# Kernel tuning notes

Hardware: AMD Instinct MI355X
Metric: run time of the kernel (lower is better)

Reference implementation:

```python
import jax, jax.numpy as jnp
import numpy as np

B, N, D, H = 256, 32768, 1024, 16
DH = D // H

def setup_inputs() -> dict:
    key = jax.random.key(0)
    ks = jax.random.split(key, 6)
    scale = 1.0 / np.sqrt(D)  # xavier-ish scale for weights
    return {
        "q": jax.random.normal(ks[0], (B, D), jnp.float32),
        "k": jax.random.normal(ks[1], (N, D), jnp.float32),
        "v": jax.random.normal(ks[2], (N, D), jnp.float32),
        "W_q": jax.random.normal(ks[3], (D, D), jnp.float32) * scale,
        "W_k": jax.random.normal(ks[4], (D, D), jnp.float32) * scale,
        "W_v": jax.random.normal(ks[5], (D, D), jnp.float32) * scale,
    }

def reference(q, k, v, W_q, W_k, W_v):
    # nn.Linear(x) = x @ W.T (no bias)
    qh = (q @ W_q.T).reshape(B, H, DH)   # [B,H,dh]
    kh = (k @ W_k.T).reshape(N, H, DH)   # [N,H,dh]
    vh = (v @ W_v.T).reshape(N, H, DH)   # [N,H,dh]
    inv_sqrt_dh = 1.0 / np.sqrt(DH).astype(np.float32)
    # decode-style cross attention: single query per (head, batch) over N keys
    score = jnp.einsum('bhd,nhd->hbn', qh, kh) * inv_sqrt_dh  # [H,B,N]
    weights = jax.nn.softmax(score, axis=-1)                   # [H,B,N]
    # dropout is identity in eval mode
    context = jnp.einsum('hbn,nhd->bhd', weights, vh)          # [B,H,dh]
    return context.reshape(B, D)
```

## Files before the change

### kernel.cpp

```cpp
#include <hip/hip_runtime.h>
#include <hip/hip_bf16.h>

#define B_  256
#define N_  32768
#define D_  1024
#define H_  16
#define DH_ 64
#define KSPLIT 16
#define STRIPE (N_ / KSPLIT)

typedef __attribute__((ext_vector_type(8))) short bf16x8;
typedef __attribute__((ext_vector_type(4))) float f32x4;

static __device__ __forceinline__ short f2bf(float f) {
    union { __hip_bfloat16 h; short s; } u;
    u.h = __float2bfloat16(f);
    return u.s;
}

__global__ __launch_bounds__(256)
void f2b_kernel(const float* __restrict__ in, short* __restrict__ out, int n4)
{
    int i = blockIdx.x * 256 + threadIdx.x;
    if (i < n4) {
        float4 v = ((const float4*)in)[i];
        ((short4*)out)[i] = make_short4(f2bf(v.x), f2bf(v.y), f2bf(v.z), f2bf(v.w));
    }
}

template<bool SWAP>
__global__ __launch_bounds__(256, 2)
void gemm_hybrid(const float* __restrict__ P, const short* __restrict__ Qb,
                 short* __restrict__ C, int MP, int MQ, int K, int ldc, float alpha)
{
    __shared__ __align__(16) short Pf[128 * 32];
    __shared__ __align__(16) short Qs[128 * 32];

    const int tid  = threadIdx.x;
    const int wave = tid >> 6;
    const int lane = tid & 63;
    const int quad = lane >> 4;
    const int l16  = lane & 15;

    const int gp = MP >> 7, gq = MQ >> 7;
    const int bid = blockIdx.x;
    int bp, bq;
    if (gp >= 8) {
        int xcd = bid & 7, w = bid >> 3, sp = gp >> 3;
        bp = xcd * sp + w / gq;
        bq = w % gq;
    } else { bp = bid / gq; bq = bid % gq; }

    const int wm = (wave & 1) * 64;
    const int wn = (wave >> 1) * 64;

    f32x4 acc[4][4];
#pragma unroll
    for (int i = 0; i < 4; ++i)
#pragma unroll
        for (int j = 0; j < 4; ++j) acc[i][j] = (f32x4){0.f, 0.f, 0.f, 0.f};

    for (int kt = 0; kt < K; kt += 32) {
        __syncthreads();
#pragma unroll
        for (int it = 0; it < 4; ++it) {
            int s = it * 256 + tid, r = s >> 3, c4 = s & 7;
            float4 v = *(const float4*)(P + (size_t)(bp * 128 + r) * K + kt + c4 * 4);
            *(short4*)&Pf[r * 32 + c4 * 4] =
                make_short4(f2bf(v.x), f2bf(v.y), f2bf(v.z), f2bf(v.w));
        }
#pragma unroll
        for (int it = 0; it < 2; ++it) {
            int s = it * 256 + tid, r = s >> 2, c8 = s & 3;
            *(bf16x8*)&Qs[r * 32 + c8 * 8] =
                *(const bf16x8*)(Qb + (size_t)(bq * 128 + r) * K + kt + c8 * 8);
        }
        __syncthreads();

        const short* LA = SWAP ? Qs : Pf;
        const short* LB = SWAP ? Pf : Qs;
        bf16x8 af[4], bf[4];
#pragma unroll
        for (int mi = 0; mi < 4; ++mi)
            af[mi] = *(const bf16x8*)&LA[(wm + mi * 16 + l16) * 32 + quad * 8];
#pragma unroll
        for (int ni = 0; ni < 4; ++ni)
            bf[ni] = *(const bf16x8*)&LB[(wn + ni * 16 + l16) * 32 + quad * 8];
#pragma unroll
        for (int mi = 0; mi < 4; ++mi)
#pragma unroll
            for (int ni = 0; ni < 4; ++ni)
                acc[mi][ni] = __builtin_amdgcn_mfma_f32_16x16x32_bf16(
                    af[mi], bf[ni], acc[mi][ni], 0, 0, 0);
    }

    const int rb = (SWAP ? bq : bp) * 128;
    const int cb = (SWAP ? bp : bq) * 128;
#pragma unroll
    for (int mi = 0; mi < 4; ++mi)
#pragma unroll
        for (int ni = 0; ni < 4; ++ni)
#pragma unroll
            for (int reg = 0; reg < 4; ++reg) {
                int r = rb + wm + mi * 16 + quad * 4 + reg;
                int c = cb + wn + ni * 16 + l16;
                C[(size_t)r * ldc + c] = f2bf(acc[mi][ni][reg] * alpha);
            }
}

__global__ __launch_bounds__(256, 2)
void attn_kernel(const short* __restrict__ qh, const short* __restrict__ kh,
                 const short* __restrict__ vhT, float* __restrict__ partO,
                 float* __restrict__ partM, float* __restrict__ partL)
{
    const int st = blockIdx.x, qb2 = blockIdx.y, h = blockIdx.z;
    const int tid  = threadIdx.x;
    const int wave = tid >> 6;
    const int lane = tid & 63;
    const int quad = lane >> 4;
    const int l16  = lane & 15;

    __shared__ __align__(16) short Ps[4][32][72];

    const int qbase = qb2 * 128 + wave * 32;
    const int hoff  = h * DH_;

    bf16x8 qfr[2][2];
#pragma unroll
    for (int qf = 0; qf < 2; ++qf)
#pragma unroll
        for (int ks = 0; ks < 2; ++ks)
            qfr[qf][ks] = *(const bf16x8*)(qh + (size_t)(qbase + qf * 16 + l16) * D_
                                           + hoff + ks * 32 + quad * 8);

    f32x4 ofrag[2][4];
#pragma unroll
    for (int qf = 0; qf < 2; ++qf)
#pragma unroll
        for (int dt = 0; dt < 4; ++dt) ofrag[qf][dt] = (f32x4){0.f, 0.f, 0.f, 0.f};
    float m_i[2] = {-__builtin_inff(), -__builtin_inff()};
    float l_i[2] = {0.f, 0.f};

    const int n0 = st * STRIPE;

    bf16x8 akf[4][2];
#pragma unroll
    for (int kf = 0; kf < 4; ++kf)
#pragma unroll
        for (int ks = 0; ks < 2; ++ks)
            akf[kf][ks] = *(const bf16x8*)(kh + (size_t)(n0 + kf * 16 + l16) * D_
                                           + hoff + ks * 32 + quad * 8);

    for (int ch = 0; ch < STRIPE; ch += 64) {
        const int nb = n0 + ch;

        f32x4 sf[4][2];
#pragma unroll
        for (int kf = 0; kf < 4; ++kf)
#pragma unroll
            for (int qf = 0; qf < 2; ++qf) sf[kf][qf] = (f32x4){0.f, 0.f, 0.f, 0.f};
#pragma unroll
        for (int ks = 0; ks < 2; ++ks)
#pragma unroll
            for (int kf = 0; kf < 4; ++kf)
#pragma unroll
                for (int qf = 0; qf < 2; ++qf)
                    sf[kf][qf] = __builtin_amdgcn_mfma_f32_16x16x32_bf16(
                        akf[kf][ks], qfr[qf][ks], sf[kf][qf], 0, 0, 0);

        bf16x8 avf[4][2];
#pragma unroll
        for (int dt = 0; dt < 4; ++dt)
#pragma unroll
            for (int g = 0; g < 2; ++g)
                avf[dt][g] = *(const bf16x8*)(vhT + (size_t)(hoff + dt * 16 + l16) * N_
                                              + nb + g * 32 + quad * 8);

        const int nbn = (ch + 64 < STRIPE) ? nb + 64 : nb;
#pragma unroll
        for (int kf = 0; kf < 4; ++kf)
#pragma unroll
            for (int ks = 0; ks < 2; ++ks)
                akf[kf][ks] = *(const bf16x8*)(kh + (size_t)(nbn + kf * 16 + l16) * D_
                                               + hoff + ks * 32 + quad * 8);

#pragma unroll
        for (int qf = 0; qf < 2; ++qf) {
            float mx = sf[0][qf][0];
#pragma unroll
            for (int kf = 0; kf < 4; ++kf)
#pragma unroll
                for (int r = 0; r < 4; ++r) mx = fmaxf(mx, sf[kf][qf][r]);
            mx = fmaxf(mx, __shfl_xor(mx, 16));
            mx = fmaxf(mx, __shfl_xor(mx, 32));
            float mn = fmaxf(m_i[qf], mx);
            float al = __expf(m_i[qf] - mn);
            m_i[qf] = mn;
            float ps = 0.f;
#pragma unroll
            for (int kf = 0; kf < 4; ++kf) {
                float p0 = __expf(sf[kf][qf][0] - mn);
                float p1 = __expf(sf[kf][qf][1] - mn);
                float p2 = __expf(sf[kf][qf][2] - mn);
                float p3 = __expf(sf[kf][qf][3] - mn);
                ps += (p0 + p1) + (p2 + p3);
                *(short4*)&Ps[wave][qf * 16 + l16][kf * 16 + quad * 4] =
                    make_short4(f2bf(p0), f2bf(p1), f2bf(p2), f2bf(p3));
            }
            ps += __shfl_xor(ps, 16);
            ps += __shfl_xor(ps, 32);
            l_i[qf] = l_i[qf] * al + ps;
#pragma unroll
            for (int dt = 0; dt < 4; ++dt) ofrag[qf][dt] *= al;
        }

#pragma unroll
        for (int qf = 0; qf < 2; ++qf)
#pragma unroll
            for (int g = 0; g < 2; ++g) {
                bf16x8 bP = *(const bf16x8*)&Ps[wave][qf * 16 + l16][g * 32 + quad * 8];
#pragma unroll
                for (int dt = 0; dt < 4; ++dt)
                    ofrag[qf][dt] = __builtin_amdgcn_mfma_f32_16x16x32_bf16(
                        avf[dt][g], bP, ofrag[qf][dt], 0, 0, 0);
            }
    }

    const int pid = ((h * KSPLIT + st) * 2 + qb2) * 4 + wave;
#pragma unroll
    for (int qf = 0; qf < 2; ++qf)
#pragma unroll
        for (int dt = 0; dt < 4; ++dt)
            *(f32x4*)&partO[((size_t)pid * 32 + qf * 16 + l16) * 64 + dt * 16 + quad * 4]
                = ofrag[qf][dt];
    if (quad == 0) {
#pragma unroll
        for (int qf = 0; qf < 2; ++qf) {
            partM[pid * 32 + qf * 16 + l16] = m_i[qf];
            partL[pid * 32 + qf * 16 + l16] = l_i[qf];
        }
    }
}

__global__ __launch_bounds__(256)
void merge_kernel(const float* __restrict__ partO, const float* __restrict__ partM,
                  const float* __restrict__ partL, float* __restrict__ out)
{
    int idx = blockIdx.x * 256 + threadIdx.x;
    int b   = idx >> 10;
    int col = idx & 1023;
    int h   = col >> 6;
    int d   = col & 63;
    int blk32 = b >> 5, rin = b & 31;
    int qb2 = blk32 >> 2, w = blk32 & 3;

    float mmax = -__builtin_inff();
#pragma unroll
    for (int st = 0; st < KSPLIT; ++st) {
        int pid = ((h * KSPLIT + st) * 2 + qb2) * 4 + w;
        mmax = fmaxf(mmax, partM[pid * 32 + rin]);
    }
    float L = 0.f, o = 0.f;
#pragma unroll
    for (int st = 0; st < KSPLIT; ++st) {
        int pid = ((h * KSPLIT + st) * 2 + qb2) * 4 + w;
        float c = __expf(partM[pid * 32 + rin] - mmax);
        L += c * partL[pid * 32 + rin];
        o += c * partO[((size_t)pid * 32 + rin) * 64 + d];
    }
    out[idx] = o / L;
}

extern "C" void kernel_launch(void* const* d_in, const int* in_sizes, int n_in,
                              void* d_out, int out_size, void* d_ws, size_t ws_size,
                              hipStream_t stream) {
    const float* q   = (const float*)d_in[0];
    const float* k   = (const float*)d_in[1];
    const float* v   = (const float*)d_in[2];
    const float* W_q = (const float*)d_in[3];
    const float* W_k = (const float*)d_in[4];
    const float* W_v = (const float*)d_in[5];
    float* out = (float*)d_out;

    short* qh  = (short*)d_ws;
    short* kh  = qh  + (size_t)B_ * D_;
    short* vhT = kh  + (size_t)N_ * D_;
    short* Wqb = vhT + (size_t)D_ * N_;
    short* Wkb = Wqb + (size_t)D_ * D_;
    short* Wvb = Wkb + (size_t)D_ * D_;
    float* partO = (float*)(Wvb + (size_t)D_ * D_);
    float* partM = partO + (size_t)2048 * 32 * 64;
    float* partL = partM + (size_t)2048 * 32;

    dim3 blk(256);
    const int w4 = (D_ * D_) / 4;

    f2b_kernel<<<dim3(w4 / 256), blk, 0, stream>>>(W_q, Wqb, w4);
    f2b_kernel<<<dim3(w4 / 256), blk, 0, stream>>>(W_k, Wkb, w4);
    f2b_kernel<<<dim3(w4 / 256), blk, 0, stream>>>(W_v, Wvb, w4);

    gemm_hybrid<false><<<dim3(2 * 8), blk, 0, stream>>>(q, Wqb, qh, B_, D_, D_, D_, 0.125f);
    gemm_hybrid<false><<<dim3(256 * 8), blk, 0, stream>>>(k, Wkb, kh, N_, D_, D_, D_, 1.0f);
    gemm_hybrid<true><<<dim3(256 * 8), blk, 0, stream>>>(v, Wvb, vhT, N_, D_, D_, N_, 1.0f);

    attn_kernel<<<dim3(KSPLIT, 2, H_), blk, 0, stream>>>(qh, kh, vhT, partO, partM, partL);
    merge_kernel<<<dim3((B_ * D_) / 256), blk, 0, stream>>>(partO, partM, partL, out);
}
```

Before: 651.0 us.

## Use direct global-to-LDS loads in projection GEMM, exp2 softmax, double KSPLIT

The projection GEMM now issues global_load_lds DMA copies of fp32 activations and bf16 weights straight into swizzled shared memory, then converts fp32 to bf16 when reading fragments. Before, every thread loaded, converted and stored to LDS itself. The softmax folds log2(e) into the query scale and uses exp2f in the attention and merge kernels. The key split grows from 16 to 32 to put more blocks on the device. In exchange the fp32 LDS tile is twice as large, which may lower occupancy, and the merge kernel now reads twice as many partial results.

Result: slower. 694.5 us (+6.7%).

```diff
diff --git a/kernel.cpp b/kernel.cpp
--- a/kernel.cpp
+++ b/kernel.cpp
@@ -6,7 +6,7 @@
 #define D_  1024
 #define H_  16
 #define DH_ 64
-#define KSPLIT 16
+#define KSPLIT 32
 #define STRIPE (N_ / KSPLIT)
 
 typedef __attribute__((ext_vector_type(8))) short bf16x8;
@@ -16,6 +16,19 @@
     union { __hip_bfloat16 h; short s; } u;
     u.h = __float2bfloat16(f);
     return u.s;
+}
+
+static __device__ __forceinline__ bf16x8 pack8(float4 a, float4 b) {
+    bf16x8 r;
+    r[0] = f2bf(a.x); r[1] = f2bf(a.y); r[2] = f2bf(a.z); r[3] = f2bf(a.w);
+    r[4] = f2bf(b.x); r[5] = f2bf(b.y); r[6] = f2bf(b.z); r[7] = f2bf(b.w);
+    return r;
+}
+
+static __device__ __forceinline__ void gload16(const void* g, void* l) {
+    __builtin_amdgcn_global_load_lds(
+        (const __attribute__((address_space(1))) void*)g,
+        (__attribute__((address_space(3))) void*)l, 16, 0, 0);
 }
 
 __global__ __launch_bounds__(256)
@@ -33,7 +46,7 @@
 void gemm_hybrid(const float* __restrict__ P, const short* __restrict__ Qb,
                  short* __restrict__ C, int MP, int MQ, int K, int ldc, float alpha)
 {
-    __shared__ __align__(16) short Pf[128 * 32];
+    __shared__ __align__(16) float Pf[128 * 32];
     __shared__ __align__(16) short Qs[128 * 32];
 
     const int tid  = threadIdx.x;
@@ -54,6 +67,37 @@
     const int wm = (wave & 1) * 64;
     const int wn = (wave >> 1) * 64;
 
+    const char* gA[4]; char* lA[4];
+#pragma unroll
+    for (int j = 0; j < 4; ++j) {
+        int s = j * 256 + tid;
+        int r = s >> 3;
+        int c = (s & 7) ^ (r & 7);
+        gA[j] = (const char*)(P + (size_t)(bp * 128 + r) * K) + c * 16;
+        lA[j] = (char*)Pf + s * 16;
+    }
+    const char* gW[2]; char* lW[2];
+#pragma unroll
+    for (int j = 0; j < 2; ++j) {
+        int s = j * 256 + tid;
+        int r = s >> 2;
+        int c = (s & 3) ^ ((r >> 1) & 3);
+        gW[j] = (const char*)(Qb + (size_t)(bq * 128 + r) * K) + c * 16;
+        lW[j] = (char*)Qs + s * 16;
+    }
+
+    const int rowPf0 = SWAP ? wn : wm;
+    const int rowQs0 = SWAP ? wm : wn;
+    int offPf[4][2], offQs[4];
+#pragma unroll
+    for (int f = 0; f < 4; ++f) {
+        int r = rowPf0 + f * 16 + l16;
+        offPf[f][0] = (r * 8 + ((quad * 2)     ^ (r & 7))) * 16;
+        offPf[f][1] = (r * 8 + ((quad * 2 + 1) ^ (r & 7))) * 16;
+        int r2 = rowQs0 + f * 16 + l16;
+        offQs[f] = (r2 * 4 + (quad ^ ((r2 >> 1) & 3))) * 16;
+    }
+
     f32x4 acc[4][4];
 #pragma unroll
     for (int i = 0; i < 4; ++i)
@@ -63,35 +107,26 @@
     for (int kt = 0; kt < K; kt += 32) {
         __syncthreads();
 #pragma unroll
-        for (int it = 0; it < 4; ++it) {
-            int s = it * 256 + tid, r = s >> 3, c4 = s & 7;
-            float4 v = *(const float4*)(P + (size_t)(bp * 128 + r) * K + kt + c4 * 4);
-            *(short4*)&Pf[r * 32 + c4 * 4] =
-                make_short4(f2bf(v.x), f2bf(v.y), f2bf(v.z), f2bf(v.w));
+        for (int j = 0; j < 4; ++j) { gload16(gA[j], lA[j]); gA[j] += 128; }
+#pragma unroll
+        for (int j = 0; j < 2; ++j) { gload16(gW[j], lW[j]); gW[j] += 64; }
+        __syncthreads();
+
+        bf16x8 fp[4], fq[4];
+#pragma unroll
+        for (int f = 0; f < 4; ++f) {
+            float4 a = *(const float4*)((const char*)Pf + offPf[f][0]);
+            float4 b = *(const float4*)((const char*)Pf + offPf[f][1]);
+            fp[f] = pack8(a, b);
+            fq[f] = *(const bf16x8*)((const char*)Qs + offQs[f]);
         }
-#pragma unroll
-        for (int it = 0; it < 2; ++it) {
-            int s = it * 256 + tid, r = s >> 2, c8 = s & 3;
-            *(bf16x8*)&Qs[r * 32 + c8 * 8] =
-                *(const bf16x8*)(Qb + (size_t)(bq * 128 + r) * K + kt + c8 * 8);
-        }
-        __syncthreads();
-
-        const short* LA = SWAP ? Qs : Pf;
-        const short* LB = SWAP ? Pf : Qs;
-        bf16x8 af[4], bf[4];
-#pragma unroll
-        for (int mi = 0; mi < 4; ++mi)
-            af[mi] = *(const bf16x8*)&LA[(wm + mi * 16 + l16) * 32 + quad * 8];
-#pragma unroll
-        for (int ni = 0; ni < 4; ++ni)
-            bf[ni] = *(const bf16x8*)&LB[(wn + ni * 16 + l16) * 32 + quad * 8];
 #pragma unroll
         for (int mi = 0; mi < 4; ++mi)
 #pragma unroll
             for (int ni = 0; ni < 4; ++ni)
                 acc[mi][ni] = __builtin_amdgcn_mfma_f32_16x16x32_bf16(
-                    af[mi], bf[ni], acc[mi][ni], 0, 0, 0);
+                    SWAP ? fq[mi] : fp[mi], SWAP ? fp[ni] : fq[ni],
+                    acc[mi][ni], 0, 0, 0);
     }
 
     const int rb = (SWAP ? bq : bp) * 128;
@@ -194,15 +229,15 @@
             mx = fmaxf(mx, __shfl_xor(mx, 16));
             mx = fmaxf(mx, __shfl_xor(mx, 32));
             float mn = fmaxf(m_i[qf], mx);
-            float al = __expf(m_i[qf] - mn);
+            float al = exp2f(m_i[qf] - mn);
             m_i[qf] = mn;
             float ps = 0.f;
 #pragma unroll
             for (int kf = 0; kf < 4; ++kf) {
-                float p0 = __expf(sf[kf][qf][0] - mn);
-                float p1 = __expf(sf[kf][qf][1] - mn);
-                float p2 = __expf(sf[kf][qf][2] - mn);
-                float p3 = __expf(sf[kf][qf][3] - mn);
+                float p0 = exp2f(sf[kf][qf][0] - mn);
+                float p1 = exp2f(sf[kf][qf][1] - mn);
+                float p2 = exp2f(sf[kf][qf][2] - mn);
+                float p3 = exp2f(sf[kf][qf][3] - mn);
                 ps += (p0 + p1) + (p2 + p3);
                 *(short4*)&Ps[wave][qf * 16 + l16][kf * 16 + quad * 4] =
                     make_short4(f2bf(p0), f2bf(p1), f2bf(p2), f2bf(p3));
@@ -264,7 +299,7 @@
 #pragma unroll
     for (int st = 0; st < KSPLIT; ++st) {
         int pid = ((h * KSPLIT + st) * 2 + qb2) * 4 + w;
-        float c = __expf(partM[pid * 32 + rin] - mmax);
+        float c = exp2f(partM[pid * 32 + rin] - mmax);
         L += c * partL[pid * 32 + rin];
         o += c * partO[((size_t)pid * 32 + rin) * 64 + d];
     }
@@ -289,17 +324,18 @@
     short* Wkb = Wqb + (size_t)D_ * D_;
     short* Wvb = Wkb + (size_t)D_ * D_;
     float* partO = (float*)(Wvb + (size_t)D_ * D_);
-    float* partM = partO + (size_t)2048 * 32 * 64;
-    float* partL = partM + (size_t)2048 * 32;
+    float* partM = partO + (size_t)4096 * 32 * 64;
+    float* partL = partM + (size_t)4096 * 32;
 
     dim3 blk(256);
     const int w4 = (D_ * D_) / 4;
+    const float alpha_q = 0.125f * 1.4426950408889634f;
 
     f2b_kernel<<<dim3(w4 / 256), blk, 0, stream>>>(W_q, Wqb, w4);
     f2b_kernel<<<dim3(w4 / 256), blk, 0, stream>>>(W_k, Wkb, w4);
     f2b_kernel<<<dim3(w4 / 256), blk, 0, stream>>>(W_v, Wvb, w4);
 
-    gemm_hybrid<false><<<dim3(2 * 8), blk, 0, stream>>>(q, Wqb, qh, B_, D_, D_, D_, 0.125f);
+    gemm_hybrid<false><<<dim3(2 * 8), blk, 0, stream>>>(q, Wqb, qh, B_, D_, D_, D_, alpha_q);
     gemm_hybrid<false><<<dim3(256 * 8), blk, 0, stream>>>(k, Wkb, kh, N_, D_, D_, D_, 1.0f);
     gemm_hybrid<true><<<dim3(256 * 8), blk, 0, stream>>>(v, Wvb, vhT, N_, D_, D_, N_, 1.0f);
 
```
